# Kernel tuning notes

Hardware: AMD Instinct MI355X
Metric: run time of the kernel (lower is better)

The kernel has to match this reference:

```python
import jax, jax.numpy as jnp
import numpy as np

MODEL_DIM = 1024
N_Q_HEADS = 16
N_GROUPS = 4
KV_PER_Q = N_Q_HEADS // N_GROUPS        # 4
HEAD_DIM = MODEL_DIM // N_Q_HEADS       # 64
KV_HEAD_DIM = MODEL_DIM // KV_PER_Q     # 256 (per-group K/V total width = N_GROUPS*HEAD_DIM)
ROPE_THETA = 50000.0


def rope_cos_sin(seq_len, dim, dtype):
    # standard RoPE tables: [S, dim]
    inv_freq = 1.0 / (ROPE_THETA ** (jnp.arange(0, dim, 2, dtype=jnp.float32) / dim))
    freqs = jnp.arange(seq_len, dtype=jnp.float32)[:, None] * inv_freq[None, :]  # [S, dim/2]
    emb = jnp.concatenate([freqs, freqs], axis=-1)                               # [S, dim]
    return jnp.cos(emb).astype(dtype), jnp.sin(emb).astype(dtype)


def rotate_half(x):
    h = x.shape[-1] // 2
    return jnp.concatenate([-x[..., h:], x[..., :h]], axis=-1)


def setup_inputs() -> dict:
    key = jax.random.key(0)
    k0, k1, k2, k3, k4 = jax.random.split(key, 5)
    B, S = 2, 2048
    qkv_out = MODEL_DIM + 2 * KV_HEAD_DIM  # 1536
    s_in = 1.0 / np.sqrt(MODEL_DIM)
    return {
        "x": jax.random.normal(k0, (B, S, MODEL_DIM), jnp.float32),
        "W_qkv": jax.random.normal(k1, (MODEL_DIM, qkv_out), jnp.float32) * s_in,
        "b_qkv": jnp.zeros((qkv_out,), jnp.float32),
        "W_out": jax.random.normal(k2, (MODEL_DIM, MODEL_DIM), jnp.float32) * s_in,
        "b_out": jnp.zeros((MODEL_DIM,), jnp.float32),
    }


def reference(x, W_qkv, b_qkv, W_out, b_out):
    B, S, _ = x.shape
    fused = x @ W_qkv + b_qkv  # [B,S,MODEL_DIM + 2*KV_HEAD_DIM]
    q, k, v = jnp.split(fused, [MODEL_DIM, MODEL_DIM + KV_HEAD_DIM], axis=-1)

    # [B,S,(NH HD)] -> [B,NH,S,HD]
    q = q.reshape(B, S, N_Q_HEADS, HEAD_DIM).transpose(0, 2, 1, 3)
    k = k.reshape(B, S, N_GROUPS, HEAD_DIM).transpose(0, 2, 1, 3)
    v = v.reshape(B, S, N_GROUPS, HEAD_DIM).transpose(0, 2, 1, 3)

    cos, sin = rope_cos_sin(S, HEAD_DIM, x.dtype)  # [S,HD]
    cos = cos[None, None]                          # [1,1,S,HD]
    sin = sin[None, None]
    q = q * cos + rotate_half(q) * sin
    k = k * cos + rotate_half(k) * sin

    # GQA without materializing duplicated heads: group queries [B,G,R,S,HD]
    qg = q.reshape(B, N_GROUPS, KV_PER_Q, S, HEAD_DIM)
    scale = 1.0 / np.sqrt(HEAD_DIM)
    scores = jnp.einsum('bgrsh,bgth->bgrst', qg, k) * scale  # [B,G,R,S,S]
    causal = jnp.tril(jnp.ones((S, S), bool))
    scores = jnp.where(causal, scores, jnp.finfo(scores.dtype).min)
    probs = jax.nn.softmax(scores, axis=-1)
    out = jnp.einsum('bgrst,bgth->bgrsh', probs, v)          # [B,G,R,S,HD]

    # [B,G,R,S,HD] -> [B,S,MODEL_DIM]  (head index = g*R + r, matching duplicate_heads)
    out = out.reshape(B, N_Q_HEADS, S, HEAD_DIM).transpose(0, 2, 1, 3).reshape(B, S, MODEL_DIM)
    return out @ W_out + b_out
```

## Files before the change

kernel.cpp:

```cpp
#include <hip/hip_runtime.h>
#include <hip/hip_bf16.h>

typedef __attribute__((ext_vector_type(8))) short short8;
typedef __attribute__((ext_vector_type(4))) float f32x4;

__device__ __forceinline__ short tobf(float f) {
  __hip_bfloat16 h = __float2bfloat16(f);
  return *reinterpret_cast<short*>(&h);
}
__device__ __forceinline__ float frombf(short s) {
  unsigned u = ((unsigned)(unsigned short)s) << 16;
  return __uint_as_float(u);
}

__device__ __forceinline__ int swz(int row) { return (row ^ (row >> 3)) & 7; }

#define GLDS16(gp, lp) __builtin_amdgcn_global_load_lds( \
    (__attribute__((address_space(1))) void*)(gp),       \
    (__attribute__((address_space(3))) void*)(lp), 16, 0, 0)

#define QSCALE 0.18033688011112042f

__global__ __launch_bounds__(256) void prep_k(
    const float* __restrict__ x, short* __restrict__ xb,
    const float* __restrict__ Wqkv, short* __restrict__ WqkvT,
    const float* __restrict__ Wout, short* __restrict__ WoutT,
    float* __restrict__ cost, float* __restrict__ sint) {
  __shared__ float t[64][65];
  const int bx = blockIdx.x, tid = threadIdx.x;
  if (bx < 1024) {
    int base = bx * 4096 + tid * 4;
#pragma unroll
    for (int rep = 0; rep < 4; ++rep) {
      int i = base + rep * 1024;
      float4 v = *(const float4*)(x + i);
      *(short4*)(xb + i) = make_short4(tobf(v.x), tobf(v.y), tobf(v.z), tobf(v.w));
    }
  } else if (bx < 1664) {
    const float* in;
    short* out;
    int C, bb;
    if (bx < 1408) { in = Wqkv; out = WqkvT; C = 1536; bb = bx - 1024; }
    else           { in = Wout; out = WoutT; C = 1024; bb = bx - 1408; }
    const int R = 1024;
    int nc = C >> 6;
    int br = bb / nc, bc = bb % nc;
    int lr = tid >> 6, lc = tid & 63;
#pragma unroll
    for (int j = 0; j < 16; ++j) {
      int r = j * 4 + lr;
      t[r][lc] = in[(size_t)(br * 64 + r) * C + bc * 64 + lc];
    }
    __syncthreads();
#pragma unroll
    for (int j = 0; j < 16; ++j) {
      int r = j * 4 + lr;
      out[(size_t)(bc * 64 + r) * R + br * 64 + lc] = tobf(t[lc][r]);
    }
  } else {
    int t2 = (bx - 1664) * 256 + tid;
    int s = t2 >> 5, f = t2 & 31;
    float inv = __expf(-(float)f * (logf(50000.0f) / 32.0f));
    float a = (float)s * inv;
    cost[t2] = cosf(a);
    sint[t2] = sinf(a);
  }
}

template <int MODE>
__global__ __launch_bounds__(256) void gemm_k(
    const short* __restrict__ A, const short* __restrict__ Bt,
    const float* __restrict__ bias, void* __restrict__ Cout,
    int M, int N, int K,
    const float* __restrict__ cost, const float* __restrict__ sint) {
  __shared__ short As[128 * 64];
  __shared__ short Bs[64 * 64];
  const int ntile = N >> 6;
  const int bm = blockIdx.x / ntile, bn = blockIdx.x % ntile;
  const int tid = threadIdx.x, w = tid >> 6, l = tid & 63;
  const int c = l & 15, g = l >> 4;
  const int m0 = bm * 128, n0 = bn * 64;

  f32x4 acc[2][4] = {};

  for (int k0 = 0; k0 < K; k0 += 64) {
#pragma unroll
    for (int j = 0; j < 4; ++j) {
      int rb = j * 32 + w * 8;
      int row = rb + (l >> 3);
      int colel = ((l & 7) ^ swz(row)) * 8;
      GLDS16(A + (size_t)(m0 + row) * K + k0 + colel, &As[rb * 64]);
      if (j < 2) GLDS16(Bt + (size_t)(n0 + row) * K + k0 + colel, &Bs[rb * 64]);
    }
    __syncthreads();
#pragma unroll
    for (int kk = 0; kk < 2; ++kk) {
      short8 af[2], bf[4];
#pragma unroll
      for (int mi = 0; mi < 2; ++mi) {
        int row = w * 32 + mi * 16 + c;
        af[mi] = *(const short8*)&As[row * 64 + ((kk * 4 + g) ^ swz(row)) * 8];
      }
#pragma unroll
      for (int ni = 0; ni < 4; ++ni) {
        int row = ni * 16 + c;
        bf[ni] = *(const short8*)&Bs[row * 64 + ((kk * 4 + g) ^ swz(row)) * 8];
      }
#pragma unroll
      for (int mi = 0; mi < 2; ++mi)
#pragma unroll
        for (int ni = 0; ni < 4; ++ni)
          acc[mi][ni] = __builtin_amdgcn_mfma_f32_16x16x32_bf16(af[mi], bf[ni], acc[mi][ni], 0, 0, 0);
    }
    __syncthreads();
  }

#pragma unroll
  for (int mi = 0; mi < 2; ++mi)
#pragma unroll
    for (int r = 0; r < 4; ++r) {
      int m = m0 + w * 32 + mi * 16 + g * 4 + r;
      int s = m & 2047;
#pragma unroll
      for (int ni = 0; ni < 4; ++ni) {
        int n = n0 + ni * 16 + c;
        float v = acc[mi][ni][r] + bias[n];
        if (MODE == 0) {
          if (n < 1280) {
            int d = n & 63, f = d & 31;
            float cs = cost[s * 32 + f], sn = sint[s * 32 + f];
            float partner = acc[mi][ni ^ 2][r] + bias[n ^ 32];
            v = (d < 32) ? (v * cs - partner * sn) : (v * cs + partner * sn);
          }
          if (n < 1024) v *= QSCALE;
          ((short*)Cout)[(size_t)m * N + n] = tobf(v);
        } else {
          ((float*)Cout)[(size_t)m * N + n] = v;
        }
      }
    }
}

__global__ __launch_bounds__(256) void vtrans_k(const short* __restrict__ qkvb,
                                                short* __restrict__ vT) {
  __shared__ short t[64][68];
  const int bx = blockIdx.x;
  const int st = bx & 31, bg = bx >> 5;
  const int b = bg >> 2, hg = bg & 3;
  const int tid = threadIdx.x, lr = tid >> 6, lc = tid & 63;
  const size_t inbase = (size_t)(b * 2048 + st * 64) * 1536 + 1280 + hg * 64;
#pragma unroll
  for (int jj = 0; jj < 16; ++jj) {
    int r = jj * 4 + lr;
    t[r][lc] = qkvb[inbase + (size_t)r * 1536 + lc];
  }
  __syncthreads();
  const size_t outbase = (size_t)(bg * 64) * 2048 + st * 64;
#pragma unroll
  for (int jj = 0; jj < 16; ++jj) {
    int d = jj * 4 + lr;
    vT[outbase + (size_t)d * 2048 + lc] = t[lc][d];
  }
}

__global__ __launch_bounds__(256) void attn_k(const short* __restrict__ qkv,
                                              const short* __restrict__ vT,
                                              short* __restrict__ pacc,
                                              float* __restrict__ plrun) {
  __shared__ short Ks3[3][64 * 64];
  __shared__ short Vt3[3][64 * 64];
  __shared__ short Ps[4][16 * 64];

  const int bx = blockIdx.x;
  const int bh = bx & 31;
  const int prr = bx >> 5;
  const int half = prr >> 3;
  const int p = prr & 7;
  const int qtB = 15 - p;
  const int qtA = p;
  const int sB = 16 - p;
  const int kB0 = half * (qtB + 1);
  const int kA0 = half * (qtA + 1);
  const int b = bh >> 4, h = bh & 15, hg = h >> 2;
  const int tid = threadIdx.x, w = tid >> 6, l = tid & 63;
  const int c = l & 15, g = l >> 4;
  const size_t rowbase = (size_t)(b * 2048) * 1536;

  const int i0row = w * 16 + (l >> 3);
  const int i1row = w * 16 + 8 + (l >> 3);
  const int c0 = ((l & 7) ^ swz(i0row)) * 8;
  const int c1 = ((l & 7) ^ swz(i1row)) * 8;
  const size_t k0off = (size_t)i0row * 1536 + c0;
  const size_t k1off = (size_t)i1row * 1536 + c1;
  const size_t v0off = (size_t)i0row * 2048 + c0;
  const size_t v1off = (size_t)i1row * 2048 + c1;
  const int lds0 = (w * 16) * 64;
  const int lds1 = (w * 16 + 8) * 64;
  const short* kbase = qkv + rowbase + 1024 + hg * 64;
  const short* vbase_p = vT + (size_t)((b * 4 + hg) * 64) * 2048;

  short8 aqB[2][2], aqA[2][2];
#pragma unroll
  for (int set = 0; set < 2; ++set)
#pragma unroll
    for (int kk = 0; kk < 2; ++kk) {
      aqB[set][kk] = *(const short8*)(qkv + rowbase +
          (size_t)(qtB * 128 + w * 32 + set * 16 + c) * 1536 + h * 64 + kk * 32 + g * 8);
      aqA[set][kk] = *(const short8*)(qkv + rowbase +
          (size_t)(qtA * 128 + w * 32 + set * 16 + c) * 1536 + h * 64 + kk * 32 + g * 8);
    }

#define KT(i) (((i) < sB) ? (kB0 + (i)) : (kA0 + ((i) - sB)))

  {
    int t0 = KT(0), t1 = KT(1);
    GLDS16(kbase + (size_t)t0 * 98304 + k0off, &Ks3[0][lds0]);
    GLDS16(kbase + (size_t)t0 * 98304 + k1off, &Ks3[0][lds1]);
    GLDS16(vbase_p + t0 * 64 + v0off, &Vt3[0][lds0]);
    GLDS16(vbase_p + t0 * 64 + v1off, &Vt3[0][lds1]);
    GLDS16(kbase + (size_t)t1 * 98304 + k0off, &Ks3[1][lds0]);
    GLDS16(kbase + (size_t)t1 * 98304 + k1off, &Ks3[1][lds1]);
    GLDS16(vbase_p + t1 * 64 + v0off, &Vt3[1][lds0]);
    GLDS16(vbase_p + t1 * 64 + v1off, &Vt3[1][lds1]);
  }
  asm volatile("s_waitcnt vmcnt(4)" ::: "memory");
  __builtin_amdgcn_s_barrier();
  __builtin_amdgcn_sched_barrier(0);

  f32x4 acco[2][4] = {};
  float lrun[2] = {0.f, 0.f};
  short* Pw = &Ps[w][0];
  int cur = 0, s2 = 2;

#define ITER(qtc, aqc)                                                          \
  {                                                                             \
    const int kt = KT(i);                                                       \
    const bool pf2 = (i + 2 < 17);                                              \
    if (pf2) {                                                                  \
      int ktp = KT(i + 2);                                                      \
      GLDS16(kbase + (size_t)ktp * 98304 + k0off, &Ks3[s2][lds0]);              \
      GLDS16(kbase + (size_t)ktp * 98304 + k1off, &Ks3[s2][lds1]);              \
      GLDS16(vbase_p + ktp * 64 + v0off, &Vt3[s2][lds0]);                       \
      GLDS16(vbase_p + ktp * 64 + v1off, &Vt3[s2][lds1]);                       \
    }                                                                           \
    short8 bk[2][4];                                                            \
    _Pragma("unroll") for (int kk = 0; kk < 2; ++kk)                            \
      _Pragma("unroll") for (int nb = 0; nb < 4; ++nb) {                        \
        int row = nb * 16 + c;                                                  \
        bk[kk][nb] = *(const short8*)&Ks3[cur][row * 64 + ((kk * 4 + g) ^ swz(row)) * 8]; \
      }                                                                         \
    f32x4 sfr[2][4] = {};                                                       \
    __builtin_amdgcn_s_setprio(1);                                              \
    _Pragma("unroll") for (int set = 0; set < 2; ++set)                         \
      _Pragma("unroll") for (int kk = 0; kk < 2; ++kk)                          \
        _Pragma("unroll") for (int nb = 0; nb < 4; ++nb)                        \
          sfr[set][nb] = __builtin_amdgcn_mfma_f32_16x16x32_bf16(               \
              bk[kk][nb], aqc[set][kk], sfr[set][nb], 0, 0, 0);                 \
    __builtin_amdgcn_s_setprio(0);                                              \
    short8 bv[2][4];                                                            \
    _Pragma("unroll") for (int kk = 0; kk < 2; ++kk)                            \
      _Pragma("unroll") for (int nb = 0; nb < 4; ++nb) {                        \
        int row = nb * 16 + c;                                                  \
        bv[kk][nb] = *(const short8*)&Vt3[cur][row * 64 + ((kk * 4 + g) ^ swz(row)) * 8]; \
      }                                                                         \
    if (kt >= 2 * (qtc)) {                                                      \
      _Pragma("unroll") for (int set = 0; set < 2; ++set) {                     \
        int qg = (qtc)*128 + w * 32 + set * 16 + c;                             \
        _Pragma("unroll") for (int nb = 0; nb < 4; ++nb)                        \
          _Pragma("unroll") for (int r = 0; r < 4; ++r)                         \
            if (kt * 64 + nb * 16 + g * 4 + r > qg) sfr[set][nb][r] = -1e30f;   \
      }                                                                         \
    }                                                                           \
    _Pragma("unroll") for (int set = 0; set < 2; ++set) {                       \
      float rs = 0.f;                                                           \
      _Pragma("unroll") for (int nb = 0; nb < 4; ++nb)                          \
        _Pragma("unroll") for (int r = 0; r < 4; ++r) {                         \
          float pv_ = exp2f(sfr[set][nb][r]);                                   \
          sfr[set][nb][r] = pv_;                                                \
          rs += pv_;                                                            \
        }                                                                       \
      rs += __shfl_xor(rs, 16, 64);                                             \
      rs += __shfl_xor(rs, 32, 64);                                             \
      lrun[set] += rs;                                                          \
      _Pragma("unroll") for (int nb = 0; nb < 4; ++nb) {                        \
        short4 pq;                                                              \
        pq.x = tobf(sfr[set][nb][0]);                                           \
        pq.y = tobf(sfr[set][nb][1]);                                           \
        pq.z = tobf(sfr[set][nb][2]);                                           \
        pq.w = tobf(sfr[set][nb][3]);                                           \
        int pslot = (nb * 2 + (g >> 1)) ^ swz(c);                               \
        *(short4*)&Pw[c * 64 + pslot * 8 + (g & 1) * 4] = pq;                   \
      }                                                                         \
      __builtin_amdgcn_s_setprio(1);                                            \
      _Pragma("unroll") for (int kk = 0; kk < 2; ++kk) {                        \
        short8 ap = *(const short8*)&Pw[c * 64 + (((kk * 4 + g) ^ swz(c)) * 8)];\
        _Pragma("unroll") for (int nb = 0; nb < 4; ++nb)                        \
          acco[set][nb] = __builtin_amdgcn_mfma_f32_16x16x32_bf16(              \
              ap, bv[kk][nb], acco[set][nb], 0, 0, 0);                          \
      }                                                                         \
      __builtin_amdgcn_s_setprio(0);                                            \
    }                                                                           \
    if (pf2) asm volatile("s_waitcnt vmcnt(4)" ::: "memory");                   \
    else     asm volatile("s_waitcnt vmcnt(0)" ::: "memory");                   \
    __builtin_amdgcn_s_barrier();                                               \
    __builtin_amdgcn_sched_barrier(0);                                          \
    cur = (cur == 2) ? 0 : cur + 1;                                             \
    s2 = (s2 == 2) ? 0 : s2 + 1;                                                \
  }

#define STORE_PARTIAL(qtP)                                                      \
  {                                                                             \
    size_t pb = ((size_t)((bh * 16 + (qtP)) * 2 + half)) * 8192;                \
    _Pragma("unroll") for (int set = 0; set < 2; ++set) {                       \
      _Pragma("unroll") for (int nb = 0; nb < 4; ++nb)                          \
        _Pragma("unroll") for (int r = 0; r < 4; ++r) {                         \
          int row = w * 32 + set * 16 + g * 4 + r;                              \
          pacc[pb + row * 64 + nb * 16 + c] = tobf(acco[set][nb][r]);           \
          acco[set][nb][r] = 0.f;                                               \
        }                                                                       \
      if (g == 0)                                                               \
        plrun[((bh * 16 + (qtP)) * 2 + half) * 128 + w * 32 + set * 16 + c] = lrun[set]; \
      lrun[set] = 0.f;                                                          \
    }                                                                           \
  }

  int i = 0;
  for (; i < sB; ++i) ITER(qtB, aqB);
  STORE_PARTIAL(qtB);
  for (; i < 17; ++i) ITER(qtA, aqA);
  STORE_PARTIAL(qtA);

#undef ITER
#undef STORE_PARTIAL
#undef KT
}

__global__ __launch_bounds__(256) void combine_k(const short* __restrict__ pacc,
                                                 const float* __restrict__ plrun,
                                                 short* __restrict__ attnb) {
  int e = blockIdx.x * 256 + threadIdx.x;
  int d8 = e & 7;
  int t = e >> 3;
  int row = t & 127;
  int t2 = t >> 7;
  int qt = t2 & 15;
  int bh = t2 >> 4;
  size_t pb = (size_t)((bh * 16 + qt) * 2) * 8192 + row * 64 + d8 * 8;
  short8 a0 = *(const short8*)(pacc + pb);
  short8 a1 = *(const short8*)(pacc + pb + 8192);
  float l = plrun[(bh * 16 + qt) * 2 * 128 + row] +
            plrun[((bh * 16 + qt) * 2 + 1) * 128 + row];
  float li = 1.0f / l;
  int b = bh >> 4, h = bh & 15;
  int m = b * 2048 + qt * 128 + row;
  int n = h * 64 + d8 * 8;
  short8 o;
#pragma unroll
  for (int k = 0; k < 8; ++k) o[k] = tobf((frombf(a0[k]) + frombf(a1[k])) * li);
  *(short8*)(attnb + (size_t)m * 1024 + n) = o;
}

extern "C" void kernel_launch(void* const* d_in, const int* in_sizes, int n_in,
                              void* d_out, int out_size, void* d_ws, size_t ws_size,
                              hipStream_t stream) {
  const float* x    = (const float*)d_in[0];
  const float* Wqkv = (const float*)d_in[1];
  const float* bqkv = (const float*)d_in[2];
  const float* Wout = (const float*)d_in[3];
  const float* bout = (const float*)d_in[4];

  char* ws = (char*)d_ws;
  short* xb    = (short*)ws; ws += 8388608;
  short* WqkvT = (short*)ws; ws += 3145728;
  short* WoutT = (short*)ws; ws += 2097152;
  short* qkvb  = (short*)ws; ws += 12582912;
  short* attnb = (short*)ws; ws += 8388608;
  short* vTb   = (short*)ws; ws += 2097152;
  float* cost  = (float*)ws; ws += 262144;
  float* sint  = (float*)ws; ws += 262144;
  short* pacc  = (short*)ws; ws += 16777216;
  float* plrun = (float*)ws; ws += 524288;

  prep_k<<<1920, 256, 0, stream>>>(x, xb, Wqkv, WqkvT, Wout, WoutT, cost, sint);
  gemm_k<0><<<768, 256, 0, stream>>>(xb, WqkvT, bqkv, (void*)qkvb, 4096, 1536, 1024, cost, sint);
  vtrans_k<<<256, 256, 0, stream>>>(qkvb, vTb);
  attn_k<<<512, 256, 0, stream>>>(qkvb, vTb, pacc, plrun);
  combine_k<<<2048, 256, 0, stream>>>(pacc, plrun, attnb);
  gemm_k<1><<<512, 256, 0, stream>>>(attnb, WoutT, bout, d_out, 4096, 1024, 1024, cost, sint);
}
```

Measured before the change: 109.3 us.

## Fuse V transpose into QKV GEMM and split attention into four key chunks

```diff
diff --git a/kernel.cpp b/kernel.cpp
--- a/kernel.cpp
+++ b/kernel.cpp
@@ -71,6 +71,7 @@
 __global__ __launch_bounds__(256) void gemm_k(
     const short* __restrict__ A, const short* __restrict__ Bt,
     const float* __restrict__ bias, void* __restrict__ Cout,
+    short* __restrict__ vT,
     int M, int N, int K,
     const float* __restrict__ cost, const float* __restrict__ sint) {
   __shared__ short As[128 * 64];
@@ -115,6 +116,27 @@
     __syncthreads();
   }
 
+  if (MODE == 0 && n0 >= 1280) {
+    const int hg = (n0 - 1280) >> 6;
+#pragma unroll
+    for (int mi = 0; mi < 2; ++mi) {
+      int m0r = m0 + w * 32 + mi * 16 + g * 4;
+      int b = m0r >> 11, s = m0r & 2047;
+#pragma unroll
+      for (int ni = 0; ni < 4; ++ni) {
+        int d = ni * 16 + c;
+        float bs = bias[n0 + d];
+        short4 o;
+        o.x = tobf(acc[mi][ni][0] + bs);
+        o.y = tobf(acc[mi][ni][1] + bs);
+        o.z = tobf(acc[mi][ni][2] + bs);
+        o.w = tobf(acc[mi][ni][3] + bs);
+        *(short4*)&vT[(size_t)((b * 4 + hg) * 64 + d) * 2048 + s] = o;
+      }
+    }
+    return;
+  }
+
 #pragma unroll
   for (int mi = 0; mi < 2; ++mi)
 #pragma unroll
@@ -126,12 +148,10 @@
         int n = n0 + ni * 16 + c;
         float v = acc[mi][ni][r] + bias[n];
         if (MODE == 0) {
-          if (n < 1280) {
-            int d = n & 63, f = d & 31;
-            float cs = cost[s * 32 + f], sn = sint[s * 32 + f];
-            float partner = acc[mi][ni ^ 2][r] + bias[n ^ 32];
-            v = (d < 32) ? (v * cs - partner * sn) : (v * cs + partner * sn);
-          }
+          int d = n & 63, f = d & 31;
+          float cs = cost[s * 32 + f], sn = sint[s * 32 + f];
+          float partner = acc[mi][ni ^ 2][r] + bias[n ^ 32];
+          v = (d < 32) ? (v * cs - partner * sn) : (v * cs + partner * sn);
           if (n < 1024) v *= QSCALE;
           ((short*)Cout)[(size_t)m * N + n] = tobf(v);
         } else {
@@ -141,46 +161,23 @@
     }
 }
 
-__global__ __launch_bounds__(256) void vtrans_k(const short* __restrict__ qkvb,
-                                                short* __restrict__ vT) {
-  __shared__ short t[64][68];
-  const int bx = blockIdx.x;
-  const int st = bx & 31, bg = bx >> 5;
-  const int b = bg >> 2, hg = bg & 3;
-  const int tid = threadIdx.x, lr = tid >> 6, lc = tid & 63;
-  const size_t inbase = (size_t)(b * 2048 + st * 64) * 1536 + 1280 + hg * 64;
-#pragma unroll
-  for (int jj = 0; jj < 16; ++jj) {
-    int r = jj * 4 + lr;
-    t[r][lc] = qkvb[inbase + (size_t)r * 1536 + lc];
-  }
-  __syncthreads();
-  const size_t outbase = (size_t)(bg * 64) * 2048 + st * 64;
-#pragma unroll
-  for (int jj = 0; jj < 16; ++jj) {
-    int d = jj * 4 + lr;
-    vT[outbase + (size_t)d * 2048 + lc] = t[lc][d];
-  }
-}
-
 __global__ __launch_bounds__(256) void attn_k(const short* __restrict__ qkv,
                                               const short* __restrict__ vT,
                                               short* __restrict__ pacc,
                                               float* __restrict__ plrun) {
-  __shared__ short Ks3[3][64 * 64];
-  __shared__ short Vt3[3][64 * 64];
+  __shared__ short Ks2[2][64 * 64];
+  __shared__ short Vt2[2][64 * 64];
   __shared__ short Ps[4][16 * 64];
 
   const int bx = blockIdx.x;
   const int bh = bx & 31;
-  const int prr = bx >> 5;
-  const int half = prr >> 3;
-  const int p = prr & 7;
-  const int qtB = 15 - p;
-  const int qtA = p;
-  const int sB = 16 - p;
-  const int kB0 = half * (qtB + 1);
-  const int kA0 = half * (qtA + 1);
+  const int rest = bx >> 5;
+  const int p = rest & 7;
+  const int ci = rest >> 3;
+  const int qtB = 15 - p, qtA = p;
+  const int sB = 32 - 2 * p;
+  const int start = (ci < 2) ? ci * 9 : 18 + (ci - 2) * 8;
+  const int end = (ci < 2) ? start + 9 : start + 8;
   const int b = bh >> 4, h = bh & 15, hg = h >> 2;
   const int tid = threadIdx.x, w = tid >> 6, l = tid & 63;
   const int c = l & 15, g = l >> 4;
@@ -199,55 +196,47 @@
   const short* kbase = qkv + rowbase + 1024 + hg * 64;
   const short* vbase_p = vT + (size_t)((b * 4 + hg) * 64) * 2048;
 
-  short8 aqB[2][2], aqA[2][2];
-#pragma unroll
-  for (int set = 0; set < 2; ++set)
-#pragma unroll
-    for (int kk = 0; kk < 2; ++kk) {
-      aqB[set][kk] = *(const short8*)(qkv + rowbase +
-          (size_t)(qtB * 128 + w * 32 + set * 16 + c) * 1536 + h * 64 + kk * 32 + g * 8);
-      aqA[set][kk] = *(const short8*)(qkv + rowbase +
-          (size_t)(qtA * 128 + w * 32 + set * 16 + c) * 1536 + h * 64 + kk * 32 + g * 8);
-    }
-
-#define KT(i) (((i) < sB) ? (kB0 + (i)) : (kA0 + ((i) - sB)))
+#define KTOF(i) (((i) < sB) ? (i) : ((i) - sB))
 
   {
-    int t0 = KT(0), t1 = KT(1);
-    GLDS16(kbase + (size_t)t0 * 98304 + k0off, &Ks3[0][lds0]);
-    GLDS16(kbase + (size_t)t0 * 98304 + k1off, &Ks3[0][lds1]);
-    GLDS16(vbase_p + t0 * 64 + v0off, &Vt3[0][lds0]);
-    GLDS16(vbase_p + t0 * 64 + v1off, &Vt3[0][lds1]);
-    GLDS16(kbase + (size_t)t1 * 98304 + k0off, &Ks3[1][lds0]);
-    GLDS16(kbase + (size_t)t1 * 98304 + k1off, &Ks3[1][lds1]);
-    GLDS16(vbase_p + t1 * 64 + v0off, &Vt3[1][lds0]);
-    GLDS16(vbase_p + t1 * 64 + v1off, &Vt3[1][lds1]);
-  }
-  asm volatile("s_waitcnt vmcnt(4)" ::: "memory");
+    int kt0 = KTOF(start);
+    GLDS16(kbase + (size_t)kt0 * 98304 + k0off, &Ks2[0][lds0]);
+    GLDS16(kbase + (size_t)kt0 * 98304 + k1off, &Ks2[0][lds1]);
+    GLDS16(vbase_p + kt0 * 64 + v0off, &Vt2[0][lds0]);
+    GLDS16(vbase_p + kt0 * 64 + v1off, &Vt2[0][lds1]);
+  }
+  asm volatile("s_waitcnt vmcnt(0)" ::: "memory");
   __builtin_amdgcn_s_barrier();
   __builtin_amdgcn_sched_barrier(0);
 
   f32x4 acco[2][4] = {};
   float lrun[2] = {0.f, 0.f};
   short* Pw = &Ps[w][0];
-  int cur = 0, s2 = 2;
-
-#define ITER(qtc, aqc)                                                          \
+  short8 aq[2][2];
+
+#pragma unroll
+  for (int set = 0; set < 2; ++set)
+#pragma unroll
+    for (int kk = 0; kk < 2; ++kk)
+      aq[set][kk] = *(const short8*)(qkv + rowbase +
+          (size_t)(qtB * 128 + w * 32 + set * 16 + c) * 1536 + h * 64 + kk * 32 + g * 8);
+
+#define BODY(qtc)                                                               \
   {                                                                             \
-    const int kt = KT(i);                                                       \
-    const bool pf2 = (i + 2 < 17);                                              \
-    if (pf2) {                                                                  \
-      int ktp = KT(i + 2);                                                      \
-      GLDS16(kbase + (size_t)ktp * 98304 + k0off, &Ks3[s2][lds0]);              \
-      GLDS16(kbase + (size_t)ktp * 98304 + k1off, &Ks3[s2][lds1]);              \
-      GLDS16(vbase_p + ktp * 64 + v0off, &Vt3[s2][lds0]);                       \
-      GLDS16(vbase_p + ktp * 64 + v1off, &Vt3[s2][lds1]);                       \
+    const int cur = (i - start) & 1, nxt = cur ^ 1;                             \
+    const int kt = KTOF(i);                                                     \
+    if (i + 1 < end) {                         \
+      int kt2 = KTOF(i + 1);                                                    \
+      GLDS16(kbase + (size_t)kt2 * 98304 + k0off, &Ks2[nxt][lds0]);             \
+      GLDS16(kbase + (size_t)kt2 * 98304 + k1off, &Ks2[nxt][lds1]);             \
+      GLDS16(vbase_p + kt2 * 64 + v0off, &Vt2[nxt][lds0]);                      \
+      GLDS16(vbase_p + kt2 * 64 + v1off, &Vt2[nxt][lds1]);                      \
     }                                                                           \
     short8 bk[2][4];                                                            \
     _Pragma("unroll") for (int kk = 0; kk < 2; ++kk)                            \
       _Pragma("unroll") for (int nb = 0; nb < 4; ++nb) {                        \
         int row = nb * 16 + c;                                                  \
-        bk[kk][nb] = *(const short8*)&Ks3[cur][row * 64 + ((kk * 4 + g) ^ swz(row)) * 8]; \
+        bk[kk][nb] = *(const short8*)&Ks2[cur][row * 64 + ((kk * 4 + g) ^ swz(row)) * 8]; \
       }                                                                         \
     f32x4 sfr[2][4] = {};                                                       \
     __builtin_amdgcn_s_setprio(1);                                              \
@@ -255,15 +244,15 @@
       _Pragma("unroll") for (int kk = 0; kk < 2; ++kk)                          \
         _Pragma("unroll") for (int nb = 0; nb < 4; ++nb)                        \
           sfr[set][nb] = __builtin_amdgcn_mfma_f32_16x16x32_bf16(               \
-              bk[kk][nb], aqc[set][kk], sfr[set][nb], 0, 0, 0);                 \
+              bk[kk][nb], aq[set][kk], sfr[set][nb], 0, 0, 0);                  \
     __builtin_amdgcn_s_setprio(0);                                              \
     short8 bv[2][4];                                                            \
     _Pragma("unroll") for (int kk = 0; kk < 2; ++kk)                            \
       _Pragma("unroll") for (int nb = 0; nb < 4; ++nb) {                        \
         int row = nb * 16 + c;                                                  \
-        bv[kk][nb] = *(const short8*)&Vt3[cur][row * 64 + ((kk * 4 + g) ^ swz(row)) * 8]; \
-      }                                                                         \
-    if (kt >= 2 * (qtc)) {                                                      \
+        bv[kk][nb] = *(const short8*)&Vt2[cur][row * 64 + ((kk * 4 + g) ^ swz(row)) * 8]; \
+      }                                                                         \
+    if (kt >= 2 * (qtc)) {            \
       _Pragma("unroll") for (int set = 0; set < 2; ++set) {                     \
         int qg = (qtc)*128 + w * 32 + set * 16 + c;                             \
         _Pragma("unroll") for (int nb = 0; nb < 4; ++nb)                        \
@@ -300,17 +289,15 @@
       }                                                                         \
       __builtin_amdgcn_s_setprio(0);                                            \
     }                                                                           \
-    if (pf2) asm volatile("s_waitcnt vmcnt(4)" ::: "memory");                   \
-    else     asm volatile("s_waitcnt vmcnt(0)" ::: "memory");                   \
+    asm volatile("s_waitcnt vmcnt(0)" ::: "memory");                            \
     __builtin_amdgcn_s_barrier();                                               \
     __builtin_amdgcn_sched_barrier(0);                                          \
-    cur = (cur == 2) ? 0 : cur + 1;                                             \
-    s2 = (s2 == 2) ? 0 : s2 + 1;                                                \
-  }
-
-#define STORE_PARTIAL(qtP)                                                      \
+  }
+
+#define STORE_PARTIAL(slot)                                                     \
   {                                                                             \
-    size_t pb = ((size_t)((bh * 16 + (qtP)) * 2 + half)) * 8192;                \
+    size_t pb = ((size_t)(((bh * 8 + p) * 4 + ci) * 2 + (slot))) * 8192;        \
+    int lb = (((bh * 8 + p) * 4 + ci) * 2 + (slot)) * 128;                      \
     _Pragma("unroll") for (int set = 0; set < 2; ++set) {                       \
       _Pragma("unroll") for (int nb = 0; nb < 4; ++nb)                          \
         _Pragma("unroll") for (int r = 0; r < 4; ++r) {                         \
@@ -318,21 +305,29 @@
           pacc[pb + row * 64 + nb * 16 + c] = tobf(acco[set][nb][r]);           \
           acco[set][nb][r] = 0.f;                                               \
         }                                                                       \
-      if (g == 0)                                                               \
-        plrun[((bh * 16 + (qtP)) * 2 + half) * 128 + w * 32 + set * 16 + c] = lrun[set]; \
+      if (g == 0) plrun[lb + w * 32 + set * 16 + c] = lrun[set];                \
       lrun[set] = 0.f;                                                          \
     }                                                                           \
   }
 
-  int i = 0;
-  for (; i < sB; ++i) ITER(qtB, aqB);
-  STORE_PARTIAL(qtB);
-  for (; i < 17; ++i) ITER(qtA, aqA);
-  STORE_PARTIAL(qtA);
-
-#undef ITER
+  int i = start;
+  const int endB = (end < sB) ? end : sB;
+  for (; i < endB; ++i) BODY(qtB);
+  STORE_PARTIAL(0);
+
+#pragma unroll
+  for (int set = 0; set < 2; ++set)
+#pragma unroll
+    for (int kk = 0; kk < 2; ++kk)
+      aq[set][kk] = *(const short8*)(qkv + rowbase +
+          (size_t)(qtA * 128 + w * 32 + set * 16 + c) * 1536 + h * 64 + kk * 32 + g * 8);
+
+  for (; i < end; ++i) BODY(qtA);
+  STORE_PARTIAL(1);
+
+#undef BODY
 #undef STORE_PARTIAL
-#undef KT
+#undef KTOF
 }
 
 __global__ __launch_bounds__(256) void combine_k(const short* __restrict__ pacc,
@@ -345,18 +340,25 @@
   int t2 = t >> 7;
   int qt = t2 & 15;
   int bh = t2 >> 4;
-  size_t pb = (size_t)((bh * 16 + qt) * 2) * 8192 + row * 64 + d8 * 8;
-  short8 a0 = *(const short8*)(pacc + pb);
-  short8 a1 = *(const short8*)(pacc + pb + 8192);
-  float l = plrun[(bh * 16 + qt) * 2 * 128 + row] +
-            plrun[((bh * 16 + qt) * 2 + 1) * 128 + row];
-  float li = 1.0f / l;
+  int p = (qt < 15 - qt) ? qt : 15 - qt;
+  int slot = (qt >= 8) ? 0 : 1;
+  float acc[8] = {};
+  float lsum = 0.f;
+#pragma unroll
+  for (int ci = 0; ci < 4; ++ci) {
+    int sidx = ((bh * 8 + p) * 4 + ci) * 2 + slot;
+    short8 a = *(const short8*)(pacc + (size_t)sidx * 8192 + row * 64 + d8 * 8);
+#pragma unroll
+    for (int k = 0; k < 8; ++k) acc[k] += frombf(a[k]);
+    lsum += plrun[sidx * 128 + row];
+  }
+  float li = 1.0f / lsum;
   int b = bh >> 4, h = bh & 15;
   int m = b * 2048 + qt * 128 + row;
   int n = h * 64 + d8 * 8;
   short8 o;
 #pragma unroll
-  for (int k = 0; k < 8; ++k) o[k] = tobf((frombf(a0[k]) + frombf(a1[k])) * li);
+  for (int k = 0; k < 8; ++k) o[k] = tobf(acc[k] * li);
   *(short8*)(attnb + (size_t)m * 1024 + n) = o;
 }
 
@@ -370,21 +372,20 @@
   const float* bout = (const float*)d_in[4];
 
   char* ws = (char*)d_ws;
-  short* xb    = (short*)ws; ws += 8388608;
-  short* WqkvT = (short*)ws; ws += 3145728;
-  short* WoutT = (short*)ws; ws += 2097152;
-  short* qkvb  = (short*)ws; ws += 12582912;
-  short* attnb = (short*)ws; ws += 8388608;
-  short* vTb   = (short*)ws; ws += 2097152;
-  float* cost  = (float*)ws; ws += 262144;
-  float* sint  = (float*)ws; ws += 262144;
-  short* pacc  = (short*)ws; ws += 16777216;
-  float* plrun = (float*)ws; ws += 524288;
+  short* pacc  = (short*)(ws + 0);
+  short* xb    = (short*)(ws + 0);
+  short* WqkvT = (short*)(ws + 8388608);
+  float* cost  = (float*)(ws + 11534336);
+  float* sint  = (float*)(ws + 11796480);
+  short* WoutT = (short*)(ws + 33554432);
+  short* qkvb  = (short*)(ws + 35651584);
+  short* attnb = (short*)(ws + 35651584);
+  short* vTb   = (short*)(ws + 48234496);
+  float* plrun = (float*)(ws + 50331648);
 
   prep_k<<<1920, 256, 0, stream>>>(x, xb, Wqkv, WqkvT, Wout, WoutT, cost, sint);
-  gemm_k<0><<<768, 256, 0, stream>>>(xb, WqkvT, bqkv, (void*)qkvb, 4096, 1536, 1024, cost, sint);
-  vtrans_k<<<256, 256, 0, stream>>>(qkvb, vTb);
-  attn_k<<<512, 256, 0, stream>>>(qkvb, vTb, pacc, plrun);
+  gemm_k<0><<<768, 256, 0, stream>>>(xb, WqkvT, bqkv, (void*)qkvb, vTb, 4096, 1536, 1024, cost, sint);
+  attn_k<<<1024, 256, 0, stream>>>(qkvb, vTb, pacc, plrun);
   combine_k<<<2048, 256, 0, stream>>>(pacc, plrun, attnb);
-  gemm_k<1><<<512, 256, 0, stream>>>(attnb, WoutT, bout, d_out, 4096, 1024, 1024, cost, sint);
-}
+  gemm_k<1><<<512, 256, 0, stream>>>(attnb, WoutT, bout, d_out, nullptr, 4096, 1024, 1024, cost, sint);
+}
```

Result: faster. 106.6 us (-2.5%).
